# Performance work log

Measured on AMD Instinct MI355X. Metric: run time of the kernel, lower is better.

The kernel has to match this reference:

```python
import jax, jax.numpy as jnp
import numpy as np

BS, L, E, H, T, V = 1024, 128, 256, 512, 20, 1000


def setup_inputs() -> dict:
    key = jax.random.key(0)
    ks = jax.random.split(key, 16)
    s = 0.05
    msg = jax.random.randint(ks[0], (BS, T), 1, V + 1)
    M = jax.random.normal(ks[1], (BS, L, E), dtype=jnp.float32)
    input_mask = jax.random.randint(ks[2], (BS, L), 0, 2) == 1
    input_mask = input_mask.at[:, 0].set(False)  # guarantee >=1 unmasked slot
    lengths = jax.random.randint(ks[3], (BS,), 0, T + 1)
    emb = jax.random.normal(ks[4], (V + 1, E), dtype=jnp.float32) * s
    Wq = jax.random.normal(ks[5], (E, H), dtype=jnp.float32) * s   # query_projection
    bq = jnp.zeros((E,), dtype=jnp.float32)
    Wc = jax.random.normal(ks[6], (H, E + H), dtype=jnp.float32) * s  # attn_combine
    bc = jnp.zeros((H,), dtype=jnp.float32)
    W_ih = jax.random.normal(ks[7], (4 * H, E), dtype=jnp.float32) * s
    W_hh = jax.random.normal(ks[8], (4 * H, H), dtype=jnp.float32) * s
    b_ih = jnp.zeros((4 * H,), dtype=jnp.float32)
    b_hh = jnp.zeros((4 * H,), dtype=jnp.float32)
    return {"msg": msg, "M": M, "input_mask": input_mask, "lengths": lengths,
            "emb": emb, "Wq": Wq, "bq": bq, "Wc": Wc, "bc": bc,
            "W_ih": W_ih, "W_hh": W_hh, "b_ih": b_ih, "b_hh": b_hh}


def _attend(h, M, input_mask, Wq, bq, Wc, bc):
    # q=(bs,H) projected to key space (bs,E); scores over L objects
    pq = h @ Wq.T + bq                                   # (bs, E)
    scores = jnp.einsum('ble,be->bl', M, pq)             # (bs, L)
    scores = jnp.where(input_mask, -jnp.inf, scores)
    w = jax.nn.softmax(scores, axis=1)                   # (bs, L)
    applied = jnp.einsum('bl,ble->be', w, M)             # (bs, E)
    att_out = jnp.concatenate([applied, h], axis=1) @ Wc.T + bc  # (bs, H)
    return att_out, w


def _lstm_cell(x, h, c, W_ih, W_hh, b_ih, b_hh):
    gates = x @ W_ih.T + b_ih + h @ W_hh.T + b_hh        # (bs, 4H)
    i, f, g, o = jnp.split(gates, 4, axis=1)
    c_new = jax.nn.sigmoid(f) * c + jax.nn.sigmoid(i) * jnp.tanh(g)
    h_new = jax.nn.sigmoid(o) * jnp.tanh(c_new)
    return h_new, c_new


def reference(msg, M, input_mask, lengths, emb, Wq, bq, Wc, bc, W_ih, W_hh, b_ih, b_hh):
    bs = msg.shape[0]
    msg_embed = emb[msg]                                 # (bs, T, E)
    xs = jnp.swapaxes(msg_embed, 0, 1)                   # (T, bs, E)
    h0 = jnp.zeros((bs, H), dtype=M.dtype)
    c0 = jnp.zeros((bs, H), dtype=M.dtype)

    def step(carry, x):
        h, c = carry
        att_out, w = _attend(h, M, input_mask, Wq, bq, Wc, bc)
        h2, c2 = _lstm_cell(x, att_out, c, W_ih, W_hh, b_ih, b_hh)
        return (h2, c2), w

    (hT, _), ws = jax.lax.scan(step, (h0, c0), xs)       # ws: (T, bs, L)
    _, w_last = _attend(hT, M, input_mask, Wq, bq, Wc, bc)
    attn_weights = jnp.swapaxes(jnp.concatenate([ws, w_last[None]], axis=0), 0, 1)  # (bs, T+1, L)
    lengths_c = jnp.clip(lengths, 0, T)
    output = attn_weights[jnp.arange(bs), lengths_c]     # (bs, L)
    logits = jnp.zeros((bs,), dtype=M.dtype)
    entropy = logits
    return (output, logits, entropy)
```

## Files before the change

### kernel.cpp

```cpp
#include <hip/hip_runtime.h>
#include <math.h>

#define NB 1024
#define L_ 128
#define E_ 256
#define H_ 512
#define T_ 20

typedef _Float16 h8 __attribute__((ext_vector_type(8)));
typedef float f4 __attribute__((ext_vector_type(4)));

__global__ __launch_bounds__(256) void detect_mask(const unsigned char* __restrict__ mask,
                                                   int* __restrict__ flag) {
    int i = blockIdx.x * 256 + threadIdx.x;
    if (mask[4 * i + 1] != 0) flag[0] = 1;
}

__global__ __launch_bounds__(256) void attend_kernel(
    const float* __restrict__ M, const unsigned char* __restrict__ maskB,
    const int* __restrict__ flag, const float* __restrict__ pq,
    const int* __restrict__ lengths, float* __restrict__ applied,
    float* __restrict__ out, int t, int writeApplied)
{
    const int b = blockIdx.x;
    const int tid = threadIdx.x;
    __shared__ float pq_s[E_];
    __shared__ float sc[L_];
    __shared__ float red[8];

    pq_s[tid] = pq[b * E_ + tid];
    __syncthreads();

    const int wave = tid >> 6, lane = tid & 63;
    const float* Mb = M + (size_t)b * L_ * E_;
    const int isByte = flag[0];
    const int* maskI = (const int*)maskB;

    for (int l = wave; l < L_; l += 4) {
        float4 mv = *reinterpret_cast<const float4*>(Mb + l * E_ + lane * 4);
        float4 pv = *reinterpret_cast<const float4*>(pq_s + lane * 4);
        float s = mv.x * pv.x + mv.y * pv.y + mv.z * pv.z + mv.w * pv.w;
        #pragma unroll
        for (int off = 32; off > 0; off >>= 1) s += __shfl_down(s, off, 64);
        if (lane == 0) {
            int msk = isByte ? (int)maskB[b * L_ + l] : maskI[b * L_ + l];
            sc[l] = msk ? -INFINITY : s;
        }
    }
    __syncthreads();

    float v = (tid < L_) ? sc[tid] : -INFINITY;
    float m = v;
    #pragma unroll
    for (int off = 32; off > 0; off >>= 1) m = fmaxf(m, __shfl_down(m, off, 64));
    if (lane == 0) red[wave] = m;
    __syncthreads();
    const float mx = fmaxf(fmaxf(red[0], red[1]), fmaxf(red[2], red[3]));
    const float e = (tid < L_) ? __expf(v - mx) : 0.0f;
    float s2 = e;
    #pragma unroll
    for (int off = 32; off > 0; off >>= 1) s2 += __shfl_down(s2, off, 64);
    if (lane == 0) red[4 + wave] = s2;
    __syncthreads();
    const float tot = red[4] + red[5] + red[6] + red[7];
    const float wgt = e / tot;
    if (tid < L_) sc[tid] = wgt;
    __syncthreads();

    int lc = lengths[b];
    lc = lc < 0 ? 0 : (lc > T_ ? T_ : lc);
    if (lc == t && tid < L_) out[(size_t)b * L_ + tid] = wgt;

    if (writeApplied) {
        float acc = 0.0f;
        #pragma unroll 8
        for (int l = 0; l < L_; ++l) acc += sc[l] * Mb[l * E_ + tid];
        applied[b * E_ + tid] = acc;
    }
}

__device__ inline void cvt8(const float4& x0, const float4& x1, h8& hi, h8& lo) {
    float xs[8] = {x0.x, x0.y, x0.z, x0.w, x1.x, x1.y, x1.z, x1.w};
    #pragma unroll
    for (int e = 0; e < 8; ++e) {
        _Float16 hh = (_Float16)xs[e];
        hi[e] = hh;
        lo[e] = (_Float16)((xs[e] - (float)hh) * 2048.0f);
    }
}

__global__ __launch_bounds__(256) void gemm_hilo(
    const float* __restrict__ A1, const float* __restrict__ A2, int K1,
    const int* __restrict__ gidx, int t,
    const float* __restrict__ B1, const float* __restrict__ B2, int BK1,
    const float* __restrict__ bias, float* __restrict__ C, int Nn, int Kn)
{
    __shared__ __align__(16) _Float16 Ah[64][40];
    __shared__ __align__(16) _Float16 Al[64][40];
    __shared__ __align__(16) _Float16 Bh[64][40];
    __shared__ __align__(16) _Float16 Bl[64][40];

    const int tid = threadIdx.x;
    const int n0 = blockIdx.x * 64, m0 = blockIdx.y * 64;
    const int lane = tid & 63, wv = tid >> 6;
    const int wr = (wv >> 1) * 32, wc = (wv & 1) * 32;
    const int fr = lane & 15, kg = (lane >> 4) * 8;
    const int sr = tid >> 2, skq = (tid & 3) * 8;

    f4 acc1[2][2] = {};
    f4 acc2[2][2] = {};
    const int KnmK1 = Kn - K1;
    const int KnmB  = Kn - BK1;

    for (int k0 = 0; k0 < Kn; k0 += 32) {
        {
            const int k = k0 + skq;
            const float* src;
            if (k < K1) {
                const int rr = gidx ? gidx[(m0 + sr) * T_ + t] : (m0 + sr);
                src = A1 + (size_t)rr * K1 + k;
            } else {
                src = A2 + (size_t)(m0 + sr) * KnmK1 + (k - K1);
            }
            float4 x0 = *reinterpret_cast<const float4*>(src);
            float4 x1 = *reinterpret_cast<const float4*>(src + 4);
            h8 hi, lo;
            cvt8(x0, x1, hi, lo);
            *reinterpret_cast<h8*>(&Ah[sr][skq]) = hi;
            *reinterpret_cast<h8*>(&Al[sr][skq]) = lo;
        }
        {
            const int k = k0 + skq;
            const float* src;
            if (k < BK1) src = B1 + (size_t)(n0 + sr) * BK1 + k;
            else         src = B2 + (size_t)(n0 + sr) * KnmB + (k - BK1);
            float4 x0 = *reinterpret_cast<const float4*>(src);
            float4 x1 = *reinterpret_cast<const float4*>(src + 4);
            h8 hi, lo;
            cvt8(x0, x1, hi, lo);
            *reinterpret_cast<h8*>(&Bh[sr][skq]) = hi;
            *reinterpret_cast<h8*>(&Bl[sr][skq]) = lo;
        }
        __syncthreads();

        h8 ah[2], al[2], bh[2], bl[2];
        #pragma unroll
        for (int i = 0; i < 2; ++i) {
            ah[i] = *reinterpret_cast<const h8*>(&Ah[wr + i * 16 + fr][kg]);
            al[i] = *reinterpret_cast<const h8*>(&Al[wr + i * 16 + fr][kg]);
            bh[i] = *reinterpret_cast<const h8*>(&Bh[wc + i * 16 + fr][kg]);
            bl[i] = *reinterpret_cast<const h8*>(&Bl[wc + i * 16 + fr][kg]);
        }
        #pragma unroll
        for (int i = 0; i < 2; ++i)
            #pragma unroll
            for (int j = 0; j < 2; ++j) {
                acc1[i][j] = __builtin_amdgcn_mfma_f32_16x16x32_f16(ah[i], bh[j], acc1[i][j], 0, 0, 0);
                acc2[i][j] = __builtin_amdgcn_mfma_f32_16x16x32_f16(ah[i], bl[j], acc2[i][j], 0, 0, 0);
                acc2[i][j] = __builtin_amdgcn_mfma_f32_16x16x32_f16(al[i], bh[j], acc2[i][j], 0, 0, 0);
            }
        __syncthreads();
    }

    const int crow0 = m0 + wr + (lane >> 4) * 4;
    const int ccol0 = n0 + wc + fr;
    #pragma unroll
    for (int i = 0; i < 2; ++i)
        #pragma unroll
        for (int j = 0; j < 2; ++j) {
            const int col = ccol0 + j * 16;
            const float bv = bias[col];
            #pragma unroll
            for (int r = 0; r < 4; ++r) {
                const int row = crow0 + i * 16 + r;
                C[(size_t)row * Nn + col] =
                    acc1[i][j][r] + acc2[i][j][r] * (1.0f / 2048.0f) + bv;
            }
        }
}

__global__ __launch_bounds__(256) void lstm_cell(
    const float* __restrict__ gates, const float* __restrict__ b_hh,
    float* __restrict__ h, float* __restrict__ c)
{
    const int idx = blockIdx.x * 256 + threadIdx.x;
    const int b = idx >> 7, q = (idx & 127) * 4;
    const float* gb = gates + (size_t)b * 2048;
    const float4 gi = *reinterpret_cast<const float4*>(gb + q);
    const float4 gf = *reinterpret_cast<const float4*>(gb + 512 + q);
    const float4 gg = *reinterpret_cast<const float4*>(gb + 1024 + q);
    const float4 go = *reinterpret_cast<const float4*>(gb + 1536 + q);
    const float4 bi = *reinterpret_cast<const float4*>(b_hh + q);
    const float4 bf = *reinterpret_cast<const float4*>(b_hh + 512 + q);
    const float4 bg = *reinterpret_cast<const float4*>(b_hh + 1024 + q);
    const float4 bo = *reinterpret_cast<const float4*>(b_hh + 1536 + q);
    const size_t hidx = (size_t)b * H_ + q;
    float4 cv = *reinterpret_cast<const float4*>(c + hidx);
    float4 hn, cn;
    const float* pi = (const float*)&gi; const float* pf = (const float*)&gf;
    const float* pg = (const float*)&gg; const float* po = (const float*)&go;
    const float* qi = (const float*)&bi; const float* qf = (const float*)&bf;
    const float* qg = (const float*)&bg; const float* qo = (const float*)&bo;
    float* pc = (float*)&cv; float* oc = (float*)&cn; float* oh = (float*)&hn;
    #pragma unroll
    for (int e = 0; e < 4; ++e) {
        const float vi = pi[e] + qi[e], vf = pf[e] + qf[e];
        const float vg = pg[e] + qg[e], vo = po[e] + qo[e];
        const float si = 1.0f / (1.0f + __expf(-vi));
        const float sf = 1.0f / (1.0f + __expf(-vf));
        const float so = 1.0f / (1.0f + __expf(-vo));
        const float tg = tanhf(vg);
        const float cnew = sf * pc[e] + si * tg;
        oc[e] = cnew;
        oh[e] = so * tanhf(cnew);
    }
    *reinterpret_cast<float4*>(c + hidx) = cn;
    *reinterpret_cast<float4*>(h + hidx) = hn;
}

extern "C" void kernel_launch(void* const* d_in, const int* in_sizes, int n_in,
                              void* d_out, int out_size, void* d_ws, size_t ws_size,
                              hipStream_t stream)
{
    const int*   msg     = (const int*)d_in[0];
    const float* M       = (const float*)d_in[1];
    const unsigned char* mask = (const unsigned char*)d_in[2];
    const int*   lengths = (const int*)d_in[3];
    const float* emb     = (const float*)d_in[4];
    const float* Wq      = (const float*)d_in[5];
    const float* bq      = (const float*)d_in[6];
    const float* Wc      = (const float*)d_in[7];
    const float* bc      = (const float*)d_in[8];
    const float* W_ih    = (const float*)d_in[9];
    const float* W_hh    = (const float*)d_in[10];
    const float* b_ih    = (const float*)d_in[11];
    const float* b_hh    = (const float*)d_in[12];
    float* out = (float*)d_out;

    float* ws      = (float*)d_ws;
    float* h       = ws;
    float* c       = ws + 524288;
    float* pq      = ws + 1048576;
    float* applied = ws + 1310720;
    float* att     = ws + 1572864;
    float* gates   = ws + 2097152;
    int*   flag    = (int*)(ws + 4194304);

    hipMemsetAsync(h, 0, 524288 * 4, stream);
    hipMemsetAsync(c, 0, 524288 * 4, stream);
    hipMemsetAsync(flag, 0, 4, stream);
    hipMemsetAsync(out + (size_t)NB * L_, 0, 2 * NB * 4, stream);

    detect_mask<<<128, 256, 0, stream>>>(mask, flag);

    for (int t = 0; t < T_; ++t) {
        gemm_hilo<<<dim3(4, 16), 256, 0, stream>>>(
            h, h, 512, nullptr, 0, Wq, Wq, 512, bq, pq, 256, 512);
        attend_kernel<<<NB, 256, 0, stream>>>(M, mask, flag, pq, lengths, applied, out, t, 1);
        gemm_hilo<<<dim3(8, 16), 256, 0, stream>>>(
            applied, h, 256, nullptr, 0, Wc, Wc, 768, bc, att, 512, 768);
        gemm_hilo<<<dim3(32, 16), 256, 0, stream>>>(
            emb, att, 256, msg, t, W_ih, W_hh, 256, b_ih, gates, 2048, 768);
        lstm_cell<<<512, 256, 0, stream>>>(gates, b_hh, h, c);
    }
    gemm_hilo<<<dim3(4, 16), 256, 0, stream>>>(
        h, h, 512, nullptr, 0, Wq, Wq, 512, bq, pq, 256, 512);
    attend_kernel<<<NB, 256, 0, stream>>>(M, mask, flag, pq, lengths, applied, out, T_, 0);
}
```

Before: 2.505 ms.

## Split attention over L into chunks with flash-style partial softmax combine

Each batch row's attention is split into four 32-row chunks, each handled by its own block. A block computes its chunk's scores, local max and exp-sum, and a partial weighted sum of M. A second kernel rescales and combines the partials into normalized weights and the applied vector. The aim is more parallelism and a shorter serial path per block in the memory-bound attention step. In exchange it adds a kernel launch per step plus extra global traffic for the partial buffers.

After: 2.436 ms. 2.8% less time.

```diff
diff --git a/kernel.cpp b/kernel.cpp
--- a/kernel.cpp
+++ b/kernel.cpp
@@ -6,6 +6,8 @@
 #define E_ 256
 #define H_ 512
 #define T_ 20
+#define CH 32
+#define NCH 4
 
 typedef _Float16 h8 __attribute__((ext_vector_type(8)));
 typedef float f4 __attribute__((ext_vector_type(4)));
@@ -16,67 +18,108 @@
     if (mask[4 * i + 1] != 0) flag[0] = 1;
 }
 
-__global__ __launch_bounds__(256) void attend_kernel(
+__global__ __launch_bounds__(256) void attend_part(
     const float* __restrict__ M, const unsigned char* __restrict__ maskB,
     const int* __restrict__ flag, const float* __restrict__ pq,
-    const int* __restrict__ lengths, float* __restrict__ applied,
-    float* __restrict__ out, int t, int writeApplied)
+    float* __restrict__ pbuf,
+    float* __restrict__ apart,
+    float2* __restrict__ stats)
+{
+    const int s = blockIdx.x, b = blockIdx.y;
+    const int tid = threadIdx.x;
+    __shared__ float pq_s[E_];
+    __shared__ float ps[CH];
+
+    pq_s[tid] = pq[b * E_ + tid];
+    __syncthreads();
+
+    const int wave = tid >> 6, lane = tid & 63;
+    const int r = lane >> 3, i = lane & 7;
+    const int l = wave * 8 + r;
+    const float* Mrow = M + ((size_t)b * L_ + s * CH + l) * E_;
+
+    float acc = 0.f;
+    #pragma unroll
+    for (int j = 0; j < 8; ++j) {
+        float4 mv = *reinterpret_cast<const float4*>(Mrow + i * 4 + j * 32);
+        float4 pv = *reinterpret_cast<const float4*>(pq_s + i * 4 + j * 32);
+        acc += mv.x * pv.x + mv.y * pv.y + mv.z * pv.z + mv.w * pv.w;
+    }
+    acc += __shfl_down(acc, 4, 64);
+    acc += __shfl_down(acc, 2, 64);
+    acc += __shfl_down(acc, 1, 64);
+
+    __shared__ float sc[CH];
+    if (i == 0) {
+        const int lg = s * CH + l;
+        int msk = flag[0] ? (int)maskB[b * L_ + lg] : ((const int*)maskB)[b * L_ + lg];
+        sc[l] = msk ? -INFINITY : acc;
+    }
+    __syncthreads();
+
+    if (wave == 0) {
+        const float v = (lane < CH) ? sc[lane] : -INFINITY;
+        float m = v;
+        #pragma unroll
+        for (int off = 32; off > 0; off >>= 1) m = fmaxf(m, __shfl_down(m, off, 64));
+        m = __shfl(m, 0, 64);
+        const float p = (lane < CH && !isinf(m)) ? __expf(v - m) : 0.f;
+        float ss = p;
+        #pragma unroll
+        for (int off = 32; off > 0; off >>= 1) ss += __shfl_down(ss, off, 64);
+        if (lane == 0) stats[b * NCH + s] = make_float2(m, ss);
+        if (lane < CH) {
+            ps[lane] = p;
+            pbuf[b * L_ + s * CH + lane] = p;
+        }
+    }
+    __syncthreads();
+
+    const float* Mc = M + ((size_t)b * L_ + s * CH) * E_;
+    float a = 0.f;
+    #pragma unroll 8
+    for (int l2 = 0; l2 < CH; ++l2) a += ps[l2] * Mc[l2 * E_ + tid];
+    apart[((size_t)b * NCH + s) * E_ + tid] = a;
+}
+
+__global__ __launch_bounds__(256) void attend_combine(
+    const float* __restrict__ pbuf, const float* __restrict__ apart,
+    const float2* __restrict__ stats, const int* __restrict__ lengths,
+    float* __restrict__ applied, float* __restrict__ out, int t, int writeApplied)
 {
     const int b = blockIdx.x;
     const int tid = threadIdx.x;
-    __shared__ float pq_s[E_];
-    __shared__ float sc[L_];
-    __shared__ float red[8];
-
-    pq_s[tid] = pq[b * E_ + tid];
+    __shared__ float scale[NCH];
+    __shared__ float zinv;
+
+    if (tid == 0) {
+        float m = -INFINITY;
+        #pragma unroll
+        for (int s = 0; s < NCH; ++s) m = fmaxf(m, stats[b * NCH + s].x);
+        float Z = 0.f;
+        #pragma unroll
+        for (int s = 0; s < NCH; ++s) {
+            const float2 st = stats[b * NCH + s];
+            const float sc = isinf(st.x) ? 0.f : __expf(st.x - m);
+            scale[s] = sc;
+            Z += st.y * sc;
+        }
+        zinv = 1.f / Z;
+    }
     __syncthreads();
 
-    const int wave = tid >> 6, lane = tid & 63;
-    const float* Mb = M + (size_t)b * L_ * E_;
-    const int isByte = flag[0];
-    const int* maskI = (const int*)maskB;
-
-    for (int l = wave; l < L_; l += 4) {
-        float4 mv = *reinterpret_cast<const float4*>(Mb + l * E_ + lane * 4);
-        float4 pv = *reinterpret_cast<const float4*>(pq_s + lane * 4);
-        float s = mv.x * pv.x + mv.y * pv.y + mv.z * pv.z + mv.w * pv.w;
-        #pragma unroll
-        for (int off = 32; off > 0; off >>= 1) s += __shfl_down(s, off, 64);
-        if (lane == 0) {
-            int msk = isByte ? (int)maskB[b * L_ + l] : maskI[b * L_ + l];
-            sc[l] = msk ? -INFINITY : s;
-        }
-    }
-    __syncthreads();
-
-    float v = (tid < L_) ? sc[tid] : -INFINITY;
-    float m = v;
-    #pragma unroll
-    for (int off = 32; off > 0; off >>= 1) m = fmaxf(m, __shfl_down(m, off, 64));
-    if (lane == 0) red[wave] = m;
-    __syncthreads();
-    const float mx = fmaxf(fmaxf(red[0], red[1]), fmaxf(red[2], red[3]));
-    const float e = (tid < L_) ? __expf(v - mx) : 0.0f;
-    float s2 = e;
-    #pragma unroll
-    for (int off = 32; off > 0; off >>= 1) s2 += __shfl_down(s2, off, 64);
-    if (lane == 0) red[4 + wave] = s2;
-    __syncthreads();
-    const float tot = red[4] + red[5] + red[6] + red[7];
-    const float wgt = e / tot;
-    if (tid < L_) sc[tid] = wgt;
-    __syncthreads();
+    if (writeApplied) {
+        float a = 0.f;
+        #pragma unroll
+        for (int s = 0; s < NCH; ++s)
+            a += apart[((size_t)b * NCH + s) * E_ + tid] * scale[s];
+        applied[b * E_ + tid] = a * zinv;
+    }
 
     int lc = lengths[b];
     lc = lc < 0 ? 0 : (lc > T_ ? T_ : lc);
-    if (lc == t && tid < L_) out[(size_t)b * L_ + tid] = wgt;
-
-    if (writeApplied) {
-        float acc = 0.0f;
-        #pragma unroll 8
-        for (int l = 0; l < L_; ++l) acc += sc[l] * Mb[l * E_ + tid];
-        applied[b * E_ + tid] = acc;
-    }
+    if (lc == t && tid < L_)
+        out[(size_t)b * L_ + tid] = pbuf[b * L_ + tid] * scale[tid >> 5] * zinv;
 }
 
 __device__ inline void cvt8(const float4& x0, const float4& x1, h8& hi, h8& lo) {
@@ -237,14 +280,17 @@
     const float* b_hh    = (const float*)d_in[12];
     float* out = (float*)d_out;
 
-    float* ws      = (float*)d_ws;
-    float* h       = ws;
-    float* c       = ws + 524288;
-    float* pq      = ws + 1048576;
-    float* applied = ws + 1310720;
-    float* att     = ws + 1572864;
-    float* gates   = ws + 2097152;
-    int*   flag    = (int*)(ws + 4194304);
+    float*  ws      = (float*)d_ws;
+    float*  h       = ws;
+    float*  c       = ws + 524288;
+    float*  pq      = ws + 1048576;
+    float*  applied = ws + 1310720;
+    float*  att     = ws + 1572864;
+    float*  gates   = ws + 2097152;
+    int*    flag    = (int*)(ws + 4194304);
+    float*  pbuf    = ws + 4194560;
+    float*  apart   = ws + 4325632;
+    float2* stats   = (float2*)(ws + 5374208);
 
     hipMemsetAsync(h, 0, 524288 * 4, stream);
     hipMemsetAsync(c, 0, 524288 * 4, stream);
@@ -256,7 +302,10 @@
     for (int t = 0; t < T_; ++t) {
         gemm_hilo<<<dim3(4, 16), 256, 0, stream>>>(
             h, h, 512, nullptr, 0, Wq, Wq, 512, bq, pq, 256, 512);
-        attend_kernel<<<NB, 256, 0, stream>>>(M, mask, flag, pq, lengths, applied, out, t, 1);
+        attend_part<<<dim3(NCH, NB), 256, 0, stream>>>(
+            M, mask, flag, pq, pbuf, apart, stats);
+        attend_combine<<<NB, 256, 0, stream>>>(
+            pbuf, apart, stats, lengths, applied, out, t, 1);
         gemm_hilo<<<dim3(8, 16), 256, 0, stream>>>(
             applied, h, 256, nullptr, 0, Wc, Wc, 768, bc, att, 512, 768);
         gemm_hilo<<<dim3(32, 16), 256, 0, stream>>>(
@@ -265,5 +314,8 @@
     }
     gemm_hilo<<<dim3(4, 16), 256, 0, stream>>>(
         h, h, 512, nullptr, 0, Wq, Wq, 512, bq, pq, 256, 512);
-    attend_kernel<<<NB, 256, 0, stream>>>(M, mask, flag, pq, lengths, applied, out, T_, 0);
-}
+    attend_part<<<dim3(NCH, NB), 256, 0, stream>>>(
+        M, mask, flag, pq, pbuf, apart, stats);
+    attend_combine<<<NB, 256, 0, stream>>>(
+        pbuf, apart, stats, lengths, applied, out, T_, 0);
+}
```
